# Optimization experiments

Hardware: AMD Instinct MI355X
Metric: run time of the kernel (lower is better)

Reference implementation:

```python
import jax, jax.numpy as jnp
import numpy as np

R2PI = float(np.sqrt(2.0 * np.pi))


def setup_inputs() -> dict:
    key = jax.random.key(0)
    k1, k2, k3 = jax.random.split(key, 3)
    B, T, D = 32, 512, 384
    feats = jax.random.normal(k1, (B, T, D), dtype=jnp.float32)
    # per-token Gaussian widths (positive, ~0.1..4.1 frames)
    rng = jax.random.uniform(k2, (B, T), dtype=jnp.float32) * 4.0 + 0.1
    # per-token durations in frames, 1..8
    durations = jax.random.randint(k3, (B, T), 1, 9, dtype=jnp.int32)
    # outlen = durations.sum(1).max() (torch uses .item(); static here)
    outlen = int(jnp.max(jnp.sum(durations, axis=1)))
    return {"feats": feats, "rng": rng, "durations": durations, "outlen": outlen}


def reference(feats, rng, durations, outlen):
    # feats: [B, T, D], rng: [B, T], durations: [B, T] int, outlen: python int
    d = durations.astype(feats.dtype)                     # [B, T]
    c = d / 2 + jnp.cumsum(d, axis=-1)                    # [B, T] gaussian centers
    r = rng + 1e-6                                        # [B, T]
    t = jnp.arange(outlen, dtype=feats.dtype)             # [outlen]
    # weights: [B, outlen, T]
    z = (t[None, :, None] - c[:, None, :]) / r[:, None, :]
    weights = jnp.exp(-0.5 * z * z) / (r[:, None, :] * R2PI) + 1e-6
    weights_normalized = weights / jnp.sum(weights, axis=2, keepdims=True)
    upsampled = jnp.matmul(weights_normalized, feats)     # [B, outlen, D]
    return upsampled
```

## Files before the change

kernel.cpp:

```cpp
#include <hip/hip_runtime.h>
#include <math.h>

#define BB 32
#define TT 512
#define DD 384
#define ROWS 48
#define WS 72
#define R2PI_INV 0.3989422804014327f
#define BAND 33.0f

typedef short bf16x8 __attribute__((ext_vector_type(8)));
typedef float f32x4  __attribute__((ext_vector_type(4)));

__device__ __forceinline__ ushort f2bf(float f) {
    unsigned u = __float_as_uint(f);
    u += 0x7fffu + ((u >> 16) & 1u);
    return (ushort)(u >> 16);
}

__global__ __launch_bounds__(256)
void prep_transpose_kernel(const float* __restrict__ feats,
                           const float* __restrict__ rng,
                           const int*   __restrict__ dur,
                           ushort* __restrict__ featsT,
                           float* __restrict__ cW,
                           float* __restrict__ irW,
                           float* __restrict__ colsumP)
{
    __shared__ unsigned sT[64 * 33];
    __shared__ float scs[256 * 4];
    const int tid = threadIdx.x;
    const int t0 = blockIdx.x * 64, d0 = blockIdx.y * 64, b = blockIdx.z;

    if (blockIdx.x == 0 && blockIdx.y == 0 && tid < 64) {
        const int ln = tid;
        int4   da = ((const int4*)(dur + b * TT))[2 * ln];
        int4   db = ((const int4*)(dur + b * TT))[2 * ln + 1];
        float4 ra = ((const float4*)(rng + b * TT))[2 * ln];
        float4 rb = ((const float4*)(rng + b * TT))[2 * ln + 1];
        int   d8[8] = {da.x, da.y, da.z, da.w, db.x, db.y, db.z, db.w};
        float r8[8] = {ra.x, ra.y, ra.z, ra.w, rb.x, rb.y, rb.z, rb.w};
        int s8 = 0;
        #pragma unroll
        for (int j = 0; j < 8; ++j) s8 += d8[j];
        int p = s8;
        #pragma unroll
        for (int off = 1; off < 64; off <<= 1) {
            int n = __shfl_up(p, off);
            if (ln >= off) p += n;
        }
        int run = p - s8;
        float c8[8], i8[8];
        #pragma unroll
        for (int j = 0; j < 8; ++j) {
            run += d8[j];
            c8[j] = 0.5f * (float)d8[j] + (float)run;
            i8[j] = 1.0f / (r8[j] + 1e-6f);
        }
        float4* cO = (float4*)(cW + b * TT + 8 * ln);
        cO[0] = (float4){c8[0], c8[1], c8[2], c8[3]};
        cO[1] = (float4){c8[4], c8[5], c8[6], c8[7]};
        float4* iO = (float4*)(irW + b * TT + 8 * ln);
        iO[0] = (float4){i8[0], i8[1], i8[2], i8[3]};
        iO[1] = (float4){i8[4], i8[5], i8[6], i8[7]};
    }

    const float4* src = (const float4*)(feats + ((size_t)b * TT + t0) * DD + d0);
    float4 csum = {0.f, 0.f, 0.f, 0.f};
    #pragma unroll
    for (int it = 0; it < 4; ++it) {
        int idx = it * 256 + tid;
        int t = idx >> 4, fq = idx & 15;
        float4 v = src[(size_t)t * (DD / 4) + fq];
        csum.x += v.x; csum.y += v.y; csum.z += v.z; csum.w += v.w;
        sT[t * 33 + 2 * fq]     = (unsigned)f2bf(v.x) | ((unsigned)f2bf(v.y) << 16);
        sT[t * 33 + 2 * fq + 1] = (unsigned)f2bf(v.z) | ((unsigned)f2bf(v.w) << 16);
    }
    *(float4*)&scs[tid * 4] = csum;
    __syncthreads();
    const ushort* sU = (const ushort*)sT;
    #pragma unroll
    for (int it = 0; it < 2; ++it) {
        int idx = it * 256 + tid;
        int d = idx >> 3, tk = idx & 7;
        unsigned r[8];
        #pragma unroll
        for (int i = 0; i < 8; ++i) r[i] = sU[(8 * tk + i) * 66 + d];
        uint4 pk;
        pk.x = r[0] | (r[1] << 16);
        pk.y = r[2] | (r[3] << 16);
        pk.z = r[4] | (r[5] << 16);
        pk.w = r[6] | (r[7] << 16);
        *(uint4*)(featsT + ((size_t)(b * DD + d0 + d)) * TT + t0 + 8 * tk) = pk;
    }
    if (tid < 64) {
        int fq = tid >> 2, j = tid & 3;
        float sum = 0.f;
        #pragma unroll
        for (int trow = 0; trow < 16; ++trow) sum += scs[(trow * 16 + fq) * 4 + j];
        colsumP[((size_t)blockIdx.x * BB + b) * DD + d0 + 4 * fq + j] = sum;
    }
}

__global__ __launch_bounds__(256)
void gemm_kernel(const ushort* __restrict__ featsT,
                 const float*  __restrict__ cW,
                 const float*  __restrict__ irW,
                 const float*  __restrict__ colsumP,
                 float* __restrict__ out, int O, int OB)
{
    __shared__ ushort sW[ROWS * WS];
    __shared__ float  sInv[ROWS];

    const int tid = threadIdx.x;
    const int ln  = tid & 63, wv = tid >> 6;
    const int qd  = ln >> 4,  lm = ln & 15;

    const int id  = blockIdx.x;
    const int xcd = id & 7;
    const int s   = id >> 3;
    const int b   = (s / OB) * 8 + xcd;
    const int i0  = (s % OB) * ROWS;

    const float lo = (float)i0 - BAND;
    const float hi = (float)(i0 + ROWS - 1) + BAND;
    int cnt = 0;
    {
        const float4* cB = (const float4*)(cW + b * TT);
        float4 ca = cB[2 * ln], cb = cB[2 * ln + 1];
        float cv[8] = {ca.x, ca.y, ca.z, ca.w, cb.x, cb.y, cb.z, cb.w};
        #pragma unroll
        for (int j = 0; j < 8; ++j) {
            cnt += (cv[j] < lo) ? 1 : 0;
            cnt += (cv[j] <= hi) ? 0x10000 : 0;
        }
        #pragma unroll
        for (int off = 32; off >= 1; off >>= 1) cnt += __shfl_xor(cnt, off);
    }
    const int j_hi = cnt >> 16;
    const int j0   = (cnt & 0xffff) & ~7;
    const int nc   = (j_hi > j0) ? ((j_hi - j0 + 63) >> 6) : 0;

    f32x4 acc[3][6];
    #pragma unroll
    for (int r = 0; r < 3; ++r)
        #pragma unroll
        for (int nt = 0; nt < 6; ++nt)
            acc[r][nt] = (f32x4){0.f, 0.f, 0.f, 0.f};
    float rsum[12];
    #pragma unroll
    for (int rr = 0; rr < 12; ++rr) rsum[rr] = 0.f;

    const int colbase = wv * 96 + lm;
    const ushort* bp = featsT + ((size_t)(b * DD + colbase)) * TT;
    const float tbase = (float)(i0 + wv * 12);

    for (int kc = 0; kc < nc; ++kc) {
        const int jt0 = j0 + (kc << 6);
        int k0 = jt0 + qd * 8;       if (k0 > TT - 8) k0 = TT - 8;
        int k1 = jt0 + 32 + qd * 8;  if (k1 > TT - 8) k1 = TT - 8;
        bf16x8 Bf[12];
        #pragma unroll
        for (int nt = 0; nt < 6; ++nt) Bf[nt]     = *(const bf16x8*)(bp + (size_t)nt * 16 * TT + k0);
        #pragma unroll
        for (int nt = 0; nt < 6; ++nt) Bf[6 + nt] = *(const bf16x8*)(bp + (size_t)nt * 16 * TT + k1);

        const int jt = jt0 + ln;
        const int jc = (jt < TT) ? jt : (TT - 1);
        const float c  = cW[b * TT + jc];
        const float ir = irW[b * TT + jc];
        const float sc0 = (jt < TT) ? (ir * R2PI_INV) : 0.0f;
        float z = (tbase - c) * ir;
        ushort h[12];
        #pragma unroll
        for (int rr = 0; rr < 12; ++rr) {
            float e = __expf(-0.5f * z * z) * sc0;
            rsum[rr] += e;
            h[rr] = f2bf(e);
            z += ir;
        }
        if (kc) __syncthreads();
        #pragma unroll
        for (int rr = 0; rr < 12; ++rr) sW[(wv * 12 + rr) * WS + ln] = h[rr];
        __syncthreads();

        #pragma unroll
        for (int ks = 0; ks < 2; ++ks)
            #pragma unroll
            for (int r = 0; r < 3; ++r) {
                bf16x8 A = *(const bf16x8*)&sW[(r * 16 + lm) * WS + ks * 32 + qd * 8];
                #pragma unroll
                for (int nt = 0; nt < 6; ++nt)
                    acc[r][nt] = __builtin_amdgcn_mfma_f32_16x16x32_bf16(A, Bf[ks * 6 + nt], acc[r][nt], 0, 0, 0);
            }
    }

    #pragma unroll
    for (int rr = 0; rr < 12; ++rr) {
        float t = rsum[rr];
        #pragma unroll
        for (int off = 32; off >= 1; off >>= 1) t += __shfl_xor(t, off);
        if (ln == 0) sInv[wv * 12 + rr] = 1.0f / (t + (float)TT * 1e-6f);
    }
    __syncthreads();

    float cs[6];
    #pragma unroll
    for (int nt = 0; nt < 6; ++nt) {
        const float* cp = colsumP + (size_t)b * DD + colbase + nt * 16;
        float t = 0.f;
        #pragma unroll
        for (int sl = 0; sl < 8; ++sl) t += cp[(size_t)sl * BB * DD];
        cs[nt] = 1e-6f * t;
    }
    #pragma unroll
    for (int r = 0; r < 3; ++r) {
        #pragma unroll
        for (int reg = 0; reg < 4; ++reg) {
            int lrow = r * 16 + qd * 4 + reg;
            int grow = i0 + lrow;
            if (grow < O) {
                float scl = sInv[lrow];
                float* op = out + ((size_t)b * O + grow) * DD + colbase;
                #pragma unroll
                for (int nt = 0; nt < 6; ++nt)
                    op[nt * 16] = (acc[r][nt][reg] + cs[nt]) * scl;
            }
        }
    }
}

extern "C" void kernel_launch(void* const* d_in, const int* in_sizes, int n_in,
                              void* d_out, int out_size, void* d_ws, size_t ws_size,
                              hipStream_t stream) {
    const float* feats = (const float*)d_in[0];
    const float* rng   = (const float*)d_in[1];
    const int*   dur   = (const int*)d_in[2];
    float* out = (float*)d_out;
    const int O = out_size / (BB * DD);
    const int OB = (O + ROWS - 1) / ROWS;

    ushort* featsT = (ushort*)d_ws;
    float*  cW  = (float*)((char*)d_ws + (size_t)BB * DD * TT * 2);
    float*  irW = cW + BB * TT;
    float*  colsumP = irW + BB * TT;

    dim3 tg(TT / 64, DD / 64, BB);
    prep_transpose_kernel<<<tg, 256, 0, stream>>>(feats, rng, dur, featsT, cW, irW, colsumP);
    gemm_kernel<<<OB * BB, 256, 0, stream>>>(featsT, cW, irW, colsumP, out, O, OB);
}
```

Baseline: 161.3 us.

## Stage GEMM epilogue through LDS for vectorized nontemporal stores and cache colsums

The epilogue now writes each 16-row accumulator slab into shared memory, then re-reads it so every thread issues contiguous 16-byte nontemporal stores, instead of scattered scalar stores with a 16-float stride. The per-column partial-sum reduction is computed once per block into shared memory and read back, rather than each thread doing eight strided global loads. The shared buffer is reused between the weight tile and the output staging, which adds extra barriers. nc is forced to at least one, so the main loop always runs, presumably so sW writes and barriers happen before the reuse.

```diff
diff --git a/kernel.cpp b/kernel.cpp
--- a/kernel.cpp
+++ b/kernel.cpp
@@ -109,8 +109,11 @@
                  const float*  __restrict__ colsumP,
                  float* __restrict__ out, int O, int OB)
 {
-    __shared__ ushort sW[ROWS * WS];
-    __shared__ float  sInv[ROWS];
+    __shared__ __align__(16) char smem[16 * 388 * 4];
+    __shared__ float sInv[ROWS];
+    ushort* sW  = (ushort*)smem;
+    float*  sC  = (float*)smem;
+    float*  sCS = (float*)(smem + 8192);
 
     const int tid = threadIdx.x;
     const int ln  = tid & 63, wv = tid >> 6;
@@ -121,6 +124,13 @@
     const int s   = id >> 3;
     const int b   = (s / OB) * 8 + xcd;
     const int i0  = (s % OB) * ROWS;
+
+    for (int idx = tid; idx < DD; idx += 256) {
+        float t = 0.f;
+        #pragma unroll
+        for (int sl = 0; sl < 8; ++sl) t += colsumP[((size_t)sl * BB + b) * DD + idx];
+        sCS[idx] = t * 1e-6f;
+    }
 
     const float lo = (float)i0 - BAND;
     const float hi = (float)(i0 + ROWS - 1) + BAND;
@@ -139,7 +149,8 @@
     }
     const int j_hi = cnt >> 16;
     const int j0   = (cnt & 0xffff) & ~7;
-    const int nc   = (j_hi > j0) ? ((j_hi - j0 + 63) >> 6) : 0;
+    int nc = (j_hi > j0) ? ((j_hi - j0 + 63) >> 6) : 0;
+    if (nc < 1) nc = 1;
 
     f32x4 acc[3][6];
     #pragma unroll
@@ -202,29 +213,34 @@
         for (int off = 32; off >= 1; off >>= 1) t += __shfl_xor(t, off);
         if (ln == 0) sInv[wv * 12 + rr] = 1.0f / (t + (float)TT * 1e-6f);
     }
+
+    float csr[6];
+    #pragma unroll
+    for (int nt = 0; nt < 6; ++nt) csr[nt] = sCS[colbase + nt * 16];
     __syncthreads();
 
-    float cs[6];
-    #pragma unroll
-    for (int nt = 0; nt < 6; ++nt) {
-        const float* cp = colsumP + (size_t)b * DD + colbase + nt * 16;
-        float t = 0.f;
-        #pragma unroll
-        for (int sl = 0; sl < 8; ++sl) t += cp[(size_t)sl * BB * DD];
-        cs[nt] = 1e-6f * t;
-    }
     #pragma unroll
     for (int r = 0; r < 3; ++r) {
+        if (r) __syncthreads();
         #pragma unroll
         for (int reg = 0; reg < 4; ++reg) {
-            int lrow = r * 16 + qd * 4 + reg;
-            int grow = i0 + lrow;
+            int lrow = qd * 4 + reg;
+            #pragma unroll
+            for (int nt = 0; nt < 6; ++nt)
+                sC[lrow * 388 + colbase + nt * 16] = acc[r][nt][reg] + csr[nt];
+        }
+        __syncthreads();
+        const int grow0 = i0 + r * 16;
+        #pragma unroll
+        for (int q = 0; q < 6; ++q) {
+            int f = q * 256 + tid;
+            int row = f / 96, c4 = f - row * 96;
+            int grow = grow0 + row;
             if (grow < O) {
-                float scl = sInv[lrow];
-                float* op = out + ((size_t)b * O + grow) * DD + colbase;
-                #pragma unroll
-                for (int nt = 0; nt < 6; ++nt)
-                    op[nt * 16] = (acc[r][nt][reg] + cs[nt]) * scl;
+                f32x4 v = *(const f32x4*)&sC[row * 388 + c4 * 4];
+                float scl = sInv[r * 16 + row];
+                v *= scl;
+                __builtin_nontemporal_store(v, (f32x4*)(out + ((size_t)b * O + grow) * DD + c4 * 4));
             }
         }
     }
```

Result: slower. 168.3 us (+4.3%).

## Store bf16 features in k-packed blocked layout and simplify prep kernel

Applied to the files above, without the earlier changes.

The prep kernel no longer transposes through shared memory. Each thread owns one feature column and writes groups of 8 consecutive tokens as packed bf16 into a [B][T/8][D][8] layout, so the GEMM's B-fragment loads for adjacent columns become contiguous. The column-sum reduction moves into the GEMM prologue (16 slices staged in shared memory), and the chunk count is clamped to at least one. Prep reads are strided per thread but coalesced across threads. The GEMM now does extra colsum reads per block, and the smaller prep grid gives fewer blocks to hide latency.

```diff
diff --git a/kernel.cpp b/kernel.cpp
--- a/kernel.cpp
+++ b/kernel.cpp
@@ -6,6 +6,7 @@
 #define DD 384
 #define ROWS 48
 #define WS 72
+#define TSL 16
 #define R2PI_INV 0.3989422804014327f
 #define BAND 33.0f
 
@@ -18,22 +19,20 @@
     return (ushort)(u >> 16);
 }
 
-__global__ __launch_bounds__(256)
-void prep_transpose_kernel(const float* __restrict__ feats,
-                           const float* __restrict__ rng,
-                           const int*   __restrict__ dur,
-                           ushort* __restrict__ featsT,
-                           float* __restrict__ cW,
-                           float* __restrict__ irW,
-                           float* __restrict__ colsumP)
+__global__ __launch_bounds__(384)
+void prep_kernel(const float* __restrict__ feats,
+                 const float* __restrict__ rng,
+                 const int*   __restrict__ dur,
+                 ushort* __restrict__ featsT,
+                 float* __restrict__ cW,
+                 float* __restrict__ irW,
+                 float* __restrict__ colsumP)
 {
-    __shared__ unsigned sT[64 * 33];
-    __shared__ float scs[256 * 4];
     const int tid = threadIdx.x;
-    const int t0 = blockIdx.x * 64, d0 = blockIdx.y * 64, b = blockIdx.z;
-
-    if (blockIdx.x == 0 && blockIdx.y == 0 && tid < 64) {
-        const int ln = tid;
+    const int tsl = blockIdx.x, b = blockIdx.y;
+
+    if (tsl == 0 && tid >= 320) {
+        const int ln = tid - 320;
         int4   da = ((const int4*)(dur + b * TT))[2 * ln];
         int4   db = ((const int4*)(dur + b * TT))[2 * ln + 1];
         float4 ra = ((const float4*)(rng + b * TT))[2 * ln];
@@ -65,41 +64,25 @@
         iO[1] = (float4){i8[4], i8[5], i8[6], i8[7]};
     }
 
-    const float4* src = (const float4*)(feats + ((size_t)b * TT + t0) * DD + d0);
-    float4 csum = {0.f, 0.f, 0.f, 0.f};
-    #pragma unroll
-    for (int it = 0; it < 4; ++it) {
-        int idx = it * 256 + tid;
-        int t = idx >> 4, fq = idx & 15;
-        float4 v = src[(size_t)t * (DD / 4) + fq];
-        csum.x += v.x; csum.y += v.y; csum.z += v.z; csum.w += v.w;
-        sT[t * 33 + 2 * fq]     = (unsigned)f2bf(v.x) | ((unsigned)f2bf(v.y) << 16);
-        sT[t * 33 + 2 * fq + 1] = (unsigned)f2bf(v.z) | ((unsigned)f2bf(v.w) << 16);
-    }
-    *(float4*)&scs[tid * 4] = csum;
-    __syncthreads();
-    const ushort* sU = (const ushort*)sT;
-    #pragma unroll
-    for (int it = 0; it < 2; ++it) {
-        int idx = it * 256 + tid;
-        int d = idx >> 3, tk = idx & 7;
-        unsigned r[8];
-        #pragma unroll
-        for (int i = 0; i < 8; ++i) r[i] = sU[(8 * tk + i) * 66 + d];
+    const int dd    = tid;
+    const int tbase = tsl * 32;
+    const float* fp = feats + ((size_t)b * TT + tbase) * DD + dd;
+    float csum = 0.f;
+    #pragma unroll
+    for (int p = 0; p < 4; ++p) {
+        float v[8];
+        #pragma unroll
+        for (int j = 0; j < 8; ++j) v[j] = fp[(size_t)(p * 8 + j) * DD];
+        #pragma unroll
+        for (int j = 0; j < 8; ++j) csum += v[j];
         uint4 pk;
-        pk.x = r[0] | (r[1] << 16);
-        pk.y = r[2] | (r[3] << 16);
-        pk.z = r[4] | (r[5] << 16);
-        pk.w = r[6] | (r[7] << 16);
-        *(uint4*)(featsT + ((size_t)(b * DD + d0 + d)) * TT + t0 + 8 * tk) = pk;
-    }
-    if (tid < 64) {
-        int fq = tid >> 2, j = tid & 3;
-        float sum = 0.f;
-        #pragma unroll
-        for (int trow = 0; trow < 16; ++trow) sum += scs[(trow * 16 + fq) * 4 + j];
-        colsumP[((size_t)blockIdx.x * BB + b) * DD + d0 + 4 * fq + j] = sum;
-    }
+        pk.x = (unsigned)f2bf(v[0]) | ((unsigned)f2bf(v[1]) << 16);
+        pk.y = (unsigned)f2bf(v[2]) | ((unsigned)f2bf(v[3]) << 16);
+        pk.z = (unsigned)f2bf(v[4]) | ((unsigned)f2bf(v[5]) << 16);
+        pk.w = (unsigned)f2bf(v[6]) | ((unsigned)f2bf(v[7]) << 16);
+        *(uint4*)(featsT + (((size_t)b * 64 + (tbase >> 3) + p) * DD + dd) * 8) = pk;
+    }
+    colsumP[((size_t)tsl * BB + b) * DD + dd] = csum;
 }
 
 __global__ __launch_bounds__(256)
@@ -111,6 +94,7 @@
 {
     __shared__ ushort sW[ROWS * WS];
     __shared__ float  sInv[ROWS];
+    __shared__ float  sCS[DD];
 
     const int tid = threadIdx.x;
     const int ln  = tid & 63, wv = tid >> 6;
@@ -121,6 +105,13 @@
     const int s   = id >> 3;
     const int b   = (s / OB) * 8 + xcd;
     const int i0  = (s % OB) * ROWS;
+
+    for (int idx = tid; idx < DD; idx += 256) {
+        float t = 0.f;
+        #pragma unroll
+        for (int sl = 0; sl < TSL; ++sl) t += colsumP[((size_t)sl * BB + b) * DD + idx];
+        sCS[idx] = t * 1e-6f;
+    }
 
     const float lo = (float)i0 - BAND;
     const float hi = (float)(i0 + ROWS - 1) + BAND;
@@ -139,7 +130,8 @@
     }
     const int j_hi = cnt >> 16;
     const int j0   = (cnt & 0xffff) & ~7;
-    const int nc   = (j_hi > j0) ? ((j_hi - j0 + 63) >> 6) : 0;
+    int nc = (j_hi > j0) ? ((j_hi - j0 + 63) >> 6) : 0;
+    if (nc < 1) nc = 1;
 
     f32x4 acc[3][6];
     #pragma unroll
@@ -152,18 +144,18 @@
     for (int rr = 0; rr < 12; ++rr) rsum[rr] = 0.f;
 
     const int colbase = wv * 96 + lm;
-    const ushort* bp = featsT + ((size_t)(b * DD + colbase)) * TT;
+    const ushort* bp = featsT + ((size_t)b * 64 * DD + colbase) * 8;
     const float tbase = (float)(i0 + wv * 12);
 
     for (int kc = 0; kc < nc; ++kc) {
         const int jt0 = j0 + (kc << 6);
-        int k0 = jt0 + qd * 8;       if (k0 > TT - 8) k0 = TT - 8;
-        int k1 = jt0 + 32 + qd * 8;  if (k1 > TT - 8) k1 = TT - 8;
+        int kp0 = (jt0 >> 3) + qd;      if (kp0 > 63) kp0 = 63;
+        int kp1 = (jt0 >> 3) + 4 + qd;  if (kp1 > 63) kp1 = 63;
         bf16x8 Bf[12];
         #pragma unroll
-        for (int nt = 0; nt < 6; ++nt) Bf[nt]     = *(const bf16x8*)(bp + (size_t)nt * 16 * TT + k0);
-        #pragma unroll
-        for (int nt = 0; nt < 6; ++nt) Bf[6 + nt] = *(const bf16x8*)(bp + (size_t)nt * 16 * TT + k1);
+        for (int nt = 0; nt < 6; ++nt) Bf[nt]     = *(const bf16x8*)(bp + (size_t)kp0 * (DD * 8) + nt * 128);
+        #pragma unroll
+        for (int nt = 0; nt < 6; ++nt) Bf[6 + nt] = *(const bf16x8*)(bp + (size_t)kp1 * (DD * 8) + nt * 128);
 
         const int jt = jt0 + ln;
         const int jc = (jt < TT) ? jt : (TT - 1);
@@ -202,17 +194,12 @@
         for (int off = 32; off >= 1; off >>= 1) t += __shfl_xor(t, off);
         if (ln == 0) sInv[wv * 12 + rr] = 1.0f / (t + (float)TT * 1e-6f);
     }
+
+    float csr[6];
+    #pragma unroll
+    for (int nt = 0; nt < 6; ++nt) csr[nt] = sCS[colbase + nt * 16];
     __syncthreads();
 
-    float cs[6];
-    #pragma unroll
-    for (int nt = 0; nt < 6; ++nt) {
-        const float* cp = colsumP + (size_t)b * DD + colbase + nt * 16;
-        float t = 0.f;
-        #pragma unroll
-        for (int sl = 0; sl < 8; ++sl) t += cp[(size_t)sl * BB * DD];
-        cs[nt] = 1e-6f * t;
-    }
     #pragma unroll
     for (int r = 0; r < 3; ++r) {
         #pragma unroll
@@ -224,7 +211,7 @@
                 float* op = out + ((size_t)b * O + grow) * DD + colbase;
                 #pragma unroll
                 for (int nt = 0; nt < 6; ++nt)
-                    op[nt * 16] = (acc[r][nt][reg] + cs[nt]) * scl;
+                    op[nt * 16] = (acc[r][nt][reg] + csr[nt]) * scl;
             }
         }
     }
@@ -245,7 +232,7 @@
     float*  irW = cW + BB * TT;
     float*  colsumP = irW + BB * TT;
 
-    dim3 tg(TT / 64, DD / 64, BB);
-    prep_transpose_kernel<<<tg, 256, 0, stream>>>(feats, rng, dur, featsT, cW, irW, colsumP);
+    dim3 pg(TSL, BB);
+    prep_kernel<<<pg, 384, 0, stream>>>(feats, rng, dur, featsT, cW, irW, colsumP);
     gemm_kernel<<<OB * BB, 256, 0, stream>>>(featsT, cW, irW, colsumP, out, O, OB);
 }
```

New measurement: 163.4 us. Within noise of the previous version (+1.3%).
